# Kernel tuning notes

Hardware: AMD Instinct MI355X
Metric: run time of the kernel (lower is better)

Reference implementation:

```python
import jax, jax.numpy as jnp
import numpy as np


def _rank_transform_ascending(flat):
    # torch: _, idx = sort(flat, descending=False); flat[idx] = linspace(0,1,n)+1/n
    n = flat.shape[0]
    order = jnp.argsort(flat)  # ascending
    prob = jnp.linspace(0.0, 1.0, n, dtype=flat.dtype) + jnp.asarray(1.0 / n, flat.dtype)
    return jnp.zeros_like(flat).at[order].set(prob)


def corr_attention(query, key, value):
    # score[b,h,i,j] = cosine-like similarity q_i . k_j / (|q_i| |k_j|)
    score = jnp.einsum('bhid,bhjd->bhij', query, key)
    q_len = jnp.sqrt(jnp.sum(query * query, axis=-1, keepdims=True)) + 1e-5  # [b,h,s,1]
    k_len = jnp.sqrt(jnp.sum(key * key, axis=-1, keepdims=True)) + 1e-5      # [b,h,s,1]
    score = score / (q_len * jnp.swapaxes(k_len, -1, -2))
    signal = jnp.sign(score)
    size = score.shape
    flat = jnp.abs(score).reshape(-1)
    ranked = _rank_transform_ascending(flat)
    score = -jnp.log(ranked).reshape(size) * signal
    score = score / jnp.sum(jnp.abs(score), axis=-1, keepdims=True)
    return jnp.einsum('bhij,bhjd->bhid', score, value)


def setup_inputs() -> dict:
    key0 = jax.random.key(0)
    kq, kk, kv = jax.random.split(key0, 3)
    B, H, S, D = 4, 8, 1024, 64
    query = jax.random.normal(kq, (B, H, S, D), dtype=jnp.float32)
    key = jax.random.normal(kk, (B, H, S, D), dtype=jnp.float32)
    value = jax.random.normal(kv, (B, H, S, D), dtype=jnp.float32)
    return {"query": query, "key": key, "value": value}


def reference(query, key, value):
    # Attention.forward with mode='season'
    return corr_attention(query, key, value)
```

## Files before the change

### kernel.cpp

```cpp
#include <hip/hip_runtime.h>
#include <math.h>
#include <stdint.h>

#define S_LEN 1024
#define D_DIM 64
#define BH    32
#define KSHIFT 13
#define NBINS 130048u
#define HOT_LO 115712u
#define NHOT   14336u
#define HIST_LO 117760u
#define NHOT_H  12288u
#define NCHUNK 254
#define HBLK   256
#define INV_NM1 (1.0f/33554431.0f)
#define INV_N   (2.9802322387695312e-08f)
#define FIX_TH  1e-4f

typedef _Float16 half8 __attribute__((ext_vector_type(8)));
typedef short    short8 __attribute__((ext_vector_type(8)));
typedef float    floatx4 __attribute__((ext_vector_type(4)));

__global__ __launch_bounds__(256) void norms_kernel(
    const float* __restrict__ Q, const float* __restrict__ K,
    double* __restrict__ qinvD, double* __restrict__ kinvD,
    float* __restrict__ qinvF, float* __restrict__ kinvF) {
  int row  = blockIdx.x * 4 + (threadIdx.x >> 6);
  int lane = threadIdx.x & 63;
  const float* src; double* dstD; float* dstF; int r = row;
  if (row < BH * S_LEN) { src = Q; dstD = qinvD; dstF = qinvF; }
  else                  { src = K; dstD = kinvD; dstF = kinvF; r = row - BH * S_LEN; }
  double v = (double)src[(size_t)r * D_DIM + lane];
  double s = v * v;
  #pragma unroll
  for (int off = 32; off; off >>= 1) s += __shfl_down(s, off);
  if (lane == 0) {
    double inv = 1.0 / (sqrt(s) + 1e-5);
    dstD[r] = inv;
    dstF[r] = (float)inv;
  }
}

__device__ __forceinline__ void bf16_split(float x, short& hi, short& lo) {
  unsigned u = __float_as_uint(x);
  unsigned h = (u + 0x7FFFu + ((u >> 16) & 1u)) >> 16;
  float hf = __uint_as_float(h << 16);
  float lf = x - hf;
  hi = (short)h;
  lo = (short)(__float_as_uint(lf) >> 16);
}

__global__ __launch_bounds__(256) void qk_mfma_kernel(
    const float* __restrict__ Q, const float* __restrict__ K,
    const float* __restrict__ qinvF, const float* __restrict__ kinvF,
    float* __restrict__ score) {
  __shared__ short Qhi[64][72], Qlo[64][72];
  __shared__ short Khi[64][72], Klo[64][72];
  int bh = blockIdx.z;
  int i0 = blockIdx.y * 64;
  int j0 = blockIdx.x * 64;
  int tid = threadIdx.x;
  const float* Qb = Q + ((size_t)bh * S_LEN + i0) * D_DIM;
  const float* Kb = K + ((size_t)bh * S_LEN + j0) * D_DIM;
  #pragma unroll
  for (int l = 0; l < 4; ++l) {
    int idx4 = l * 256 + tid;
    int row  = idx4 >> 4;
    int c4   = idx4 & 15;
    float qi = qinvF[(size_t)bh * S_LEN + i0 + row];
    float4 v = ((const float4*)Qb)[idx4];
    float qv[4] = {v.x * qi, v.y * qi, v.z * qi, v.w * qi};
    short qh[4], ql[4];
    #pragma unroll
    for (int c = 0; c < 4; ++c) bf16_split(qv[c], qh[c], ql[c]);
    *(short4*)&Qhi[row][c4 * 4] = make_short4(qh[0], qh[1], qh[2], qh[3]);
    *(short4*)&Qlo[row][c4 * 4] = make_short4(ql[0], ql[1], ql[2], ql[3]);
    float kj = kinvF[(size_t)bh * S_LEN + j0 + row];
    float4 w = ((const float4*)Kb)[idx4];
    float kv[4] = {w.x * kj, w.y * kj, w.z * kj, w.w * kj};
    short kh[4], kl[4];
    #pragma unroll
    for (int c = 0; c < 4; ++c) bf16_split(kv[c], kh[c], kl[c]);
    *(short4*)&Khi[row][c4 * 4] = make_short4(kh[0], kh[1], kh[2], kh[3]);
    *(short4*)&Klo[row][c4 * 4] = make_short4(kl[0], kl[1], kl[2], kl[3]);
  }
  __syncthreads();
  int wave = tid >> 6;
  int lane = tid & 63;
  int m    = lane & 15;
  int quad = lane >> 4;
  floatx4 acc[4];
  #pragma unroll
  for (int n = 0; n < 4; ++n) acc[n] = (floatx4){0.f, 0.f, 0.f, 0.f};
  #pragma unroll
  for (int ks = 0; ks < 2; ++ks) {
    int kb = ks * 32 + quad * 8;
    short8 a_hi = *(const short8*)&Qhi[wave * 16 + m][kb];
    short8 a_lo = *(const short8*)&Qlo[wave * 16 + m][kb];
    #pragma unroll
    for (int nt = 0; nt < 4; ++nt) {
      short8 b_hi = *(const short8*)&Khi[nt * 16 + m][kb];
      short8 b_lo = *(const short8*)&Klo[nt * 16 + m][kb];
      acc[nt] = __builtin_amdgcn_mfma_f32_16x16x32_bf16(a_hi, b_hi, acc[nt], 0, 0, 0);
      acc[nt] = __builtin_amdgcn_mfma_f32_16x16x32_bf16(a_hi, b_lo, acc[nt], 0, 0, 0);
      acc[nt] = __builtin_amdgcn_mfma_f32_16x16x32_bf16(a_lo, b_hi, acc[nt], 0, 0, 0);
    }
  }
  #pragma unroll
  for (int r = 0; r < 4; ++r) {
    float* op = score + ((size_t)bh * S_LEN + i0 + wave * 16 + quad * 4 + r) * S_LEN + j0 + m;
    #pragma unroll
    for (int nt = 0; nt < 4; ++nt)
      op[nt * 16] = acc[nt][r];
  }
}

__global__ __launch_bounds__(1024) void hist_kernel(
    float* __restrict__ score, const float* __restrict__ Q, const float* __restrict__ K,
    const double* __restrict__ qinvD, const double* __restrict__ kinvD,
    unsigned* __restrict__ hist, unsigned char* __restrict__ partial) {
  __shared__ unsigned lh[NHOT_H];
  int tid = threadIdx.x;
  int lane = tid & 63;
  for (unsigned i = tid; i < NHOT_H; i += 1024) lh[i] = 0u;
  __syncthreads();
  const float4* p = (const float4*)score + (size_t)blockIdx.x * 32768;
  #pragma unroll 2
  for (int it = 0; it < 32; ++it) {
    float4 v = p[it * 1024 + tid];
    float vv[4] = {v.x, v.y, v.z, v.w};
    bool anyf = (fabsf(vv[0]) < FIX_TH) | (fabsf(vv[1]) < FIX_TH) |
                (fabsf(vv[2]) < FIX_TH) | (fabsf(vv[3]) < FIX_TH);
    unsigned long long am = __ballot(anyf);
    while (am) {
      int src = (int)(__ffsll((long long)am) - 1);
      am &= am - 1;
      unsigned base4 = (unsigned)(blockIdx.x * 32768u + (unsigned)(it * 1024 + tid));
      unsigned b4 = __shfl(base4, src);
      #pragma unroll
      for (int c = 0; c < 4; ++c) {
        float sc = __shfl(vv[c], src);
        if (fabsf(sc) < FIX_TH) {
          unsigned flat = b4 * 4u + (unsigned)c;
          unsigned bh = flat >> 20, i = (flat >> 10) & 1023u, j = flat & 1023u;
          double qd = (double)Q[((size_t)bh * S_LEN + i) * D_DIM + lane];
          double kd = (double)K[((size_t)bh * S_LEN + j) * D_DIM + lane];
          double pd = qd * kd;
          #pragma unroll
          for (int off = 32; off; off >>= 1) pd += __shfl_down(pd, off);
          float corr = 0.f;
          if (lane == 0)
            corr = (float)(pd * qinvD[(size_t)bh * S_LEN + i] * kinvD[(size_t)bh * S_LEN + j]);
          corr = __shfl(corr, 0);
          if (lane == src) {
            vv[c] = corr;
            score[(size_t)flat] = corr;
          }
        }
      }
    }
    #pragma unroll
    for (int c = 0; c < 4; ++c) {
      unsigned b = __float_as_uint(fabsf(vv[c])) >> KSHIFT;
      if (b >= NBINS) b = NBINS - 1u;
      if (b >= HIST_LO) atomicAdd(&lh[b - HIST_LO], 1u);
      else              atomicAdd(&hist[b], 1u);
    }
  }
  __syncthreads();
  unsigned char* dst = partial + (size_t)blockIdx.x * NHOT_H;
  for (unsigned i = tid; i < NHOT_H; i += 1024) dst[i] = (unsigned char)lh[i];
}

__global__ __launch_bounds__(256) void hreduce_kernel(
    const unsigned char* __restrict__ partial, unsigned* __restrict__ hist) {
  unsigned bin = blockIdx.x * 256 + threadIdx.x;
  unsigned s = 0;
  #pragma unroll 8
  for (int b = 0; b < HBLK; ++b) s += (unsigned)partial[(size_t)b * NHOT_H + bin];
  hist[HIST_LO + bin] = s;
}

__global__ __launch_bounds__(256) void vt_kernel(
    const float* __restrict__ V, _Float16* __restrict__ Vt) {
  __shared__ _Float16 T[64][72];
  int bh = blockIdx.y, j0 = blockIdx.x * 64, tid = threadIdx.x;
  const float* Vb = V + ((size_t)bh * S_LEN + j0) * D_DIM;
  #pragma unroll
  for (int l = 0; l < 4; ++l) {
    int idx = l * 256 + tid;
    int jr = idx >> 4, d4 = idx & 15;
    float4 v = ((const float4*)Vb)[idx];
    T[d4*4+0][jr] = (_Float16)v.x;
    T[d4*4+1][jr] = (_Float16)v.y;
    T[d4*4+2][jr] = (_Float16)v.z;
    T[d4*4+3][jr] = (_Float16)v.w;
  }
  __syncthreads();
  _Float16* Ob = Vt + (size_t)bh * D_DIM * S_LEN + j0;
  #pragma unroll
  for (int l = 0; l < 2; ++l) {
    int idx = l * 256 + tid;
    int d = idx >> 3, jc = idx & 7;
    uint4 val = *(const uint4*)&T[d][jc*8];
    *(uint4*)(Ob + (size_t)d * S_LEN + jc*8) = val;
  }
}

__global__ __launch_bounds__(256) void scan1_kernel(const unsigned* __restrict__ hist,
                                                    unsigned* __restrict__ csum) {
  __shared__ unsigned sd[256];
  int c = blockIdx.x, t = threadIdx.x;
  const unsigned* p = hist + (size_t)c * 512;
  sd[t] = p[t] + p[t + 256];
  __syncthreads();
  for (int off = 128; off; off >>= 1) {
    if (t < off) sd[t] += sd[t + off];
    __syncthreads();
  }
  if (t == 0) csum[c] = sd[0];
}

__global__ __launch_bounds__(256) void scan2_kernel(unsigned* __restrict__ csum) {
  __shared__ unsigned d[256];
  int t = threadIdx.x;
  unsigned v = (t < NCHUNK) ? csum[t] : 0u;
  d[t] = v; __syncthreads();
  for (int off = 1; off < 256; off <<= 1) {
    unsigned x = (t >= off) ? d[t - off] : 0u;
    __syncthreads();
    d[t] += x;
    __syncthreads();
  }
  if (t < NCHUNK) csum[t] = d[t] - v;
}

__global__ __launch_bounds__(256) void scan3_kernel(const unsigned* __restrict__ hist,
                                                    const unsigned* __restrict__ csum,
                                                    _Float16* __restrict__ tTab16) {
  __shared__ unsigned ts[256];
  int c = blockIdx.x, t = threadIdx.x;
  const unsigned* p = hist + (size_t)c * 512 + t * 2;
  unsigned l0 = p[0], l1 = p[1];
  unsigned s = l0 + l1;
  ts[t] = s; __syncthreads();
  for (int off = 1; off < 256; off <<= 1) {
    unsigned x = (t >= off) ? ts[t - off] : 0u;
    __syncthreads();
    ts[t] += x;
    __syncthreads();
  }
  unsigned base = csum[c] + ts[t] - s;
  int idx = c * 512 + t * 2;
  float r0 = (float)base + 0.5f * ((float)l0 - 1.0f);
  tTab16[idx]     = (_Float16)(-__logf(fmaf(r0, INV_NM1, INV_N)));
  float r1 = (float)(base + l0) + 0.5f * ((float)l1 - 1.0f);
  tTab16[idx + 1] = (_Float16)(-__logf(fmaf(r1, INV_NM1, INV_N)));
}

__global__ __launch_bounds__(256) void pv_mfma_kernel(
    const float* __restrict__ score, const _Float16* __restrict__ Vt,
    const unsigned short* __restrict__ tTab16, float* __restrict__ out) {
  __shared__ unsigned short ldsT[NHOT];
  int tid = threadIdx.x;
  {
    const unsigned* gsrc = (const unsigned*)(tTab16 + HOT_LO);
    unsigned* ldst = (unsigned*)ldsT;
    #pragma unroll
    for (int i = 0; i < 28; ++i)
      ldst[i * 256 + tid] = gsrc[i * 256 + tid];
  }
  __syncthreads();

  int bh   = blockIdx.y;
  int wave = tid >> 6;
  int lane = tid & 63;
  int m    = lane & 15;
  int quad = lane >> 4;
  int i0   = blockIdx.x * 64 + wave * 16;
  const float*    Sb = score + ((size_t)bh * S_LEN + i0 + m) * S_LEN;
  const _Float16* Vb = Vt + (size_t)bh * D_DIM * S_LEN;
  floatx4 acc[4];
  #pragma unroll
  for (int n = 0; n < 4; ++n) acc[n] = (floatx4){0.f, 0.f, 0.f, 0.f};
  float rsum = 0.f;

  for (int ks = 0; ks < 32; ++ks) {
    int k0 = ks * 32 + quad * 8;
    float4 s0 = *(const float4*)(Sb + k0);
    float4 s1 = *(const float4*)(Sb + k0 + 4);
    float sv[8] = {s0.x, s0.y, s0.z, s0.w, s1.x, s1.y, s1.z, s1.w};
    union { unsigned short u[8]; half8 h; } af;
    #pragma unroll
    for (int e = 0; e < 8; ++e) {
      unsigned u = __float_as_uint(sv[e]);
      unsigned a = u & 0x7fffffffu;
      unsigned b = a >> KSHIFT;
      if (b > NBINS - 1u) b = NBINS - 1u;
      unsigned short tb;
      if (b >= HOT_LO) tb = ldsT[b - HOT_LO];
      else             tb = tTab16[b];
      if (a == 0u) tb = 0;
      af.u[e] = (unsigned short)(tb ^ ((u >> 16) & 0x8000u));
      unsigned short tabs = (unsigned short)(tb & 0x7fffu);
      _Float16 th = __builtin_bit_cast(_Float16, tabs);
      rsum += (float)th;
    }
    half8 bf[4];
    #pragma unroll
    for (int n = 0; n < 4; ++n)
      bf[n] = *(const half8*)(Vb + (size_t)(n * 16 + m) * S_LEN + k0);
    #pragma unroll
    for (int n = 0; n < 4; ++n)
      acc[n] = __builtin_amdgcn_mfma_f32_16x16x32_f16(af.h, bf[n], acc[n], 0, 0, 0);
  }

  rsum += __shfl_xor(rsum, 16);
  rsum += __shfl_xor(rsum, 32);
  float inv = 1.0f / rsum;
  #pragma unroll
  for (int r = 0; r < 4; ++r) {
    int row = quad * 4 + r;
    float invr = __shfl(inv, row);
    float* op = out + ((size_t)bh * S_LEN + i0 + row) * D_DIM + m;
    #pragma unroll
    for (int n = 0; n < 4; ++n)
      op[n * 16] = acc[n][r] * invr;
  }
}

extern "C" void kernel_launch(void* const* d_in, const int* in_sizes, int n_in,
                              void* d_out, int out_size, void* d_ws, size_t ws_size,
                              hipStream_t stream) {
  const float* Q = (const float*)d_in[0];
  const float* K = (const float*)d_in[1];
  const float* V = (const float*)d_in[2];
  float* out = (float*)d_out;
  char* ws = (char*)d_ws;
  float*         score   = (float*)(ws);
  unsigned*      hist    = (unsigned*)(ws + 134217728);
  unsigned char* partial = (unsigned char*)(ws + 134737920);
  double*        qinvD   = (double*)(ws + 137883648);
  double*        kinvD   = (double*)(ws + 138145792);
  float*         qinvF   = (float*)(ws + 138407936);
  float*         kinvF   = (float*)(ws + 138539008);
  _Float16*      Vt      = (_Float16*)(ws + 134737920);
  unsigned*      csum    = (unsigned*)(ws + 139194368);
  _Float16*      tTab16  = (_Float16*)(ws + 139195392);

  hipMemsetAsync(hist, 0, NBINS * sizeof(unsigned), stream);
  norms_kernel<<<(2 * BH * S_LEN) / 4, 256, 0, stream>>>(Q, K, qinvD, kinvD, qinvF, kinvF);
  qk_mfma_kernel<<<dim3(16, 16, BH), 256, 0, stream>>>(Q, K, qinvF, kinvF, score);
  hist_kernel<<<HBLK, 1024, 0, stream>>>(score, Q, K, qinvD, kinvD, hist, partial);
  hreduce_kernel<<<NHOT_H / 256, 256, 0, stream>>>(partial, hist);
  vt_kernel<<<dim3(16, BH), 256, 0, stream>>>(V, Vt);
  scan1_kernel<<<NCHUNK, 256, 0, stream>>>(hist, csum);
  scan2_kernel<<<1, 256, 0, stream>>>(csum);
  scan3_kernel<<<NCHUNK, 256, 0, stream>>>(hist, csum, tTab16);
  pv_mfma_kernel<<<dim3(16, BH), 256, 0, stream>>>(
      score, Vt, (const unsigned short*)tTab16, out);
}
```

Baseline: 219.6 us.

## Split PV kernel reduction dimension across waves to raise block count

The PV kernel now assigns 16 query rows per block and splits the 1024-long key dimension across the four waves, with partial MFMA accumulators and row sums combined through shared memory. The grid grows from 16x32 to 64x32 blocks, aiming for better occupancy of the GPU's compute units on this memory-bound pass. To fit the extra reduction buffer in LDS, the hot table cached in shared memory shrinks, so more lookups fall back to global memory. Each block also reloads the table, which quadruples total table-staging traffic.

```diff
diff --git a/kernel.cpp b/kernel.cpp
--- a/kernel.cpp
+++ b/kernel.cpp
@@ -7,8 +7,8 @@
 #define BH    32
 #define KSHIFT 13
 #define NBINS 130048u
-#define HOT_LO 115712u
-#define NHOT   14336u
+#define PV_LO  119808u
+#define NPVT   10240u
 #define HIST_LO 117760u
 #define NHOT_H  12288u
 #define NCHUNK 254
@@ -261,13 +261,14 @@
 __global__ __launch_bounds__(256) void pv_mfma_kernel(
     const float* __restrict__ score, const _Float16* __restrict__ Vt,
     const unsigned short* __restrict__ tTab16, float* __restrict__ out) {
-  __shared__ unsigned short ldsT[NHOT];
+  __shared__ unsigned short ldsT[NPVT];
+  __shared__ float red[4352];
   int tid = threadIdx.x;
   {
-    const unsigned* gsrc = (const unsigned*)(tTab16 + HOT_LO);
+    const unsigned* gsrc = (const unsigned*)(tTab16 + PV_LO);
     unsigned* ldst = (unsigned*)ldsT;
     #pragma unroll
-    for (int i = 0; i < 28; ++i)
+    for (int i = 0; i < 20; ++i)
       ldst[i * 256 + tid] = gsrc[i * 256 + tid];
   }
   __syncthreads();
@@ -277,7 +278,7 @@
   int lane = tid & 63;
   int m    = lane & 15;
   int quad = lane >> 4;
-  int i0   = blockIdx.x * 64 + wave * 16;
+  int i0   = blockIdx.x * 16;
   const float*    Sb = score + ((size_t)bh * S_LEN + i0 + m) * S_LEN;
   const _Float16* Vb = Vt + (size_t)bh * D_DIM * S_LEN;
   floatx4 acc[4];
@@ -285,8 +286,8 @@
   for (int n = 0; n < 4; ++n) acc[n] = (floatx4){0.f, 0.f, 0.f, 0.f};
   float rsum = 0.f;
 
-  for (int ks = 0; ks < 32; ++ks) {
-    int k0 = ks * 32 + quad * 8;
+  for (int ks = 0; ks < 8; ++ks) {
+    int k0 = wave * 256 + ks * 32 + quad * 8;
     float4 s0 = *(const float4*)(Sb + k0);
     float4 s1 = *(const float4*)(Sb + k0 + 4);
     float sv[8] = {s0.x, s0.y, s0.z, s0.w, s1.x, s1.y, s1.z, s1.w};
@@ -298,8 +299,8 @@
       unsigned b = a >> KSHIFT;
       if (b > NBINS - 1u) b = NBINS - 1u;
       unsigned short tb;
-      if (b >= HOT_LO) tb = ldsT[b - HOT_LO];
-      else             tb = tTab16[b];
+      if (b >= PV_LO) tb = ldsT[b - PV_LO];
+      else            tb = tTab16[b];
       if (a == 0u) tb = 0;
       af.u[e] = (unsigned short)(tb ^ ((u >> 16) & 0x8000u));
       unsigned short tabs = (unsigned short)(tb & 0x7fffu);
@@ -315,17 +316,29 @@
       acc[n] = __builtin_amdgcn_mfma_f32_16x16x32_f16(af.h, bf[n], acc[n], 0, 0, 0);
   }
 
-  rsum += __shfl_xor(rsum, 16);
-  rsum += __shfl_xor(rsum, 32);
-  float inv = 1.0f / rsum;
-  #pragma unroll
-  for (int r = 0; r < 4; ++r) {
-    int row = quad * 4 + r;
-    float invr = __shfl(inv, row);
-    float* op = out + ((size_t)bh * S_LEN + i0 + row) * D_DIM + m;
-    #pragma unroll
-    for (int n = 0; n < 4; ++n)
-      op[n * 16] = acc[n][r] * invr;
+  #pragma unroll
+  for (int n = 0; n < 4; ++n)
+    #pragma unroll
+    for (int r = 0; r < 4; ++r)
+      red[(wave * 16 + quad * 4 + r) * 64 + n * 16 + m] = acc[n][r];
+  red[4096 + wave * 64 + lane] = rsum;
+  __syncthreads();
+
+  int col = tid & 63;
+  int rq  = tid >> 6;
+  #pragma unroll
+  for (int t = 0; t < 4; ++t) {
+    int row = rq * 4 + t;
+    float s = 0.f;
+    #pragma unroll
+    for (int w = 0; w < 4; ++w) s += red[(w * 16 + row) * 64 + col];
+    float rs = 0.f;
+    #pragma unroll
+    for (int w = 0; w < 4; ++w)
+      #pragma unroll
+      for (int q = 0; q < 4; ++q)
+        rs += red[4096 + w * 64 + q * 16 + row];
+    out[((size_t)bh * S_LEN + i0 + row) * D_DIM + col] = s / rs;
   }
 }
 
@@ -357,6 +370,6 @@
   scan1_kernel<<<NCHUNK, 256, 0, stream>>>(hist, csum);
   scan2_kernel<<<1, 256, 0, stream>>>(csum);
   scan3_kernel<<<NCHUNK, 256, 0, stream>>>(hist, csum, tTab16);
-  pv_mfma_kernel<<<dim3(16, BH), 256, 0, stream>>>(
+  pv_mfma_kernel<<<dim3(S_LEN / 16, BH), 256, 0, stream>>>(
       score, Vt, (const unsigned short*)tTab16, out);
 }
```

New measurement: 216.0 us. No clear change (-1.6%).
